# Performance work log

Hardware: AMD Instinct MI355X
Metric: run time of the kernel (lower is better)

The kernel has to match this reference:

```python
import math
import jax, jax.numpy as jnp
import numpy as np

NUM_HEAD = 8
EPS = 1e-5

def _ln(v, w, b):
    m = jnp.mean(v, axis=-1, keepdims=True)
    var = jnp.var(v, axis=-1, keepdims=True)  # biased var, as torch LayerNorm
    return (v - m) * jax.lax.rsqrt(var + EPS) * w + b

def setup_inputs() -> dict:
    key = jax.random.key(0)
    ks = jax.random.split(key, 5)
    B, T, D, L, Hd = 16, 2048, 512, 768, 512
    return {
        "x": jax.random.normal(ks[0], (B, T, D), jnp.float32),
        "xf": jax.random.normal(ks[1], (B, T, L), jnp.float32),
        "norm_w": jnp.ones((D,), jnp.float32),
        "norm_b": jnp.zeros((D,), jnp.float32),
        "tnorm_w": jnp.ones((L,), jnp.float32),
        "tnorm_b": jnp.zeros((L,), jnp.float32),
        "Wq": jax.random.normal(ks[2], (Hd, D), jnp.float32) * (1.0 / math.sqrt(D)),
        "Wk": jax.random.normal(ks[3], (Hd, L), jnp.float32) * (1.0 / math.sqrt(L)),
        "Wv": jax.random.normal(ks[4], (Hd, L), jnp.float32) * (1.0 / math.sqrt(L)),
    }

def reference(x, xf, norm_w, norm_b, tnorm_w, tnorm_b, Wq, Wk, Wv):
    B, T, _ = x.shape
    Hd = Wq.shape[0]
    H = NUM_HEAD
    d = Hd // H
    q = _ln(x, norm_w, norm_b) @ Wq.T                 # B,T,Hd
    xf_n = _ln(xf, tnorm_w, tnorm_b)
    k = xf_n @ Wk.T                                   # B,T,Hd (N == T)
    v = xf_n @ Wv.T                                   # B,T,Hd
    qh = q.reshape(B, T, H, d)
    kh = k.reshape(B, T, H, d)
    vh = v.reshape(B, T, H, d)
    # per-position, per-head dot product gate (no softmax)
    w = jnp.einsum('bthd,bthd->bth', qh, kh) / math.sqrt(d)
    # dropout in eval mode = identity
    y2 = (w[..., None] * vh).reshape(B, T, Hd)
    y1 = ((1.0 - w)[..., None] * qh).reshape(B, T, Hd)
    return (y1, y2)
```

## Files before the change

kernel.cpp:

```cpp
#include <hip/hip_runtime.h>

#define NT 512
#define MT 64

typedef __attribute__((ext_vector_type(8))) short short8;
typedef __attribute__((ext_vector_type(4))) float f32x4;
typedef __attribute__((ext_vector_type(4))) unsigned short u16x4;

__device__ __forceinline__ unsigned short f2bf(float f) {
  unsigned int u = __builtin_bit_cast(unsigned int, f);
  u += 0x7fffu + ((u >> 16) & 1u);
  return (unsigned short)(u >> 16);
}

__global__ void cvt_weights(const float* __restrict__ wq,
                            const float* __restrict__ wk,
                            const float* __restrict__ wv,
                            unsigned short* __restrict__ o) {
  int stride = gridDim.x * blockDim.x;
  int i0 = blockIdx.x * blockDim.x + threadIdx.x;
  for (int t = i0; t < 32768; t += stride) {
    int lane = t & 63, n = (t >> 6) & 3, kk32 = (t >> 8) & 15, head = t >> 12;
    int row = head * 64 + n * 16 + (lane & 15);
    int k   = kk32 * 32 + (lane >> 4) * 8;
    const float* s = wq + (size_t)row * 512 + k;
    unsigned short* d = o + (size_t)t * 8;
    #pragma unroll
    for (int e = 0; e < 8; ++e) d[e] = f2bf(s[e]);
  }
  for (int t = i0; t < 49152; t += stride) {
    int lane = t & 63, n = (t >> 6) & 3, rem = t >> 8;
    int kk32 = rem % 24, head = rem / 24;
    int row = head * 64 + n * 16 + (lane & 15);
    int k   = kk32 * 32 + (lane >> 4) * 8;
    const float* s = wk + (size_t)row * 768 + k;
    unsigned short* d = o + 262144 + (size_t)t * 8;
    #pragma unroll
    for (int e = 0; e < 8; ++e) d[e] = f2bf(s[e]);
  }
  for (int t = i0; t < 49152; t += stride) {
    int lane = t & 63, n = (t >> 6) & 3, rem = t >> 8;
    int kk32 = rem % 24, head = rem / 24;
    int row = head * 64 + n * 16 + (lane & 15);
    int k   = kk32 * 32 + (lane >> 4) * 8;
    const float* s = wv + (size_t)row * 768 + k;
    unsigned short* d = o + 655360 + (size_t)t * 8;
    #pragma unroll
    for (int e = 0; e < 8; ++e) d[e] = f2bf(s[e]);
  }
}

__global__ __launch_bounds__(NT, 2)
void fused_xattn(const float* __restrict__ x, const float* __restrict__ xf,
                 const float* __restrict__ nw, const float* __restrict__ nb,
                 const float* __restrict__ tw, const float* __restrict__ tb,
                 const unsigned short* __restrict__ wbf,
                 float* __restrict__ out) {
  __shared__ __attribute__((aligned(16))) char smem[98304];
  const int tid   = threadIdx.x;
  const int lane  = tid & 63;
  const int wid   = tid >> 6;
  const int lr    = lane & 15;
  const int lkb   = (lane >> 4) * 8;
  const int lrow4 = (lane >> 4) * 4;

  const long row0 = (long)blockIdx.x * MT;
  float* __restrict__ y1 = out;
  float* __restrict__ y2 = out + 16777216L;

  {
    f32x4 t0[8], t1[8];
    #pragma unroll
    for (int j = 0; j < 8; ++j) {
      const f32x4* rp = (const f32x4*)(x + (row0 + wid + 8 * j) * 512);
      t0[j] = rp[lane]; t1[j] = rp[lane + 64];
    }
    const f32x4* g4 = (const f32x4*)nw;
    const f32x4* b4 = (const f32x4*)nb;
    f32x4 g0 = g4[lane], g1 = g4[lane + 64];
    f32x4 c0 = b4[lane], c1 = b4[lane + 64];
    #pragma unroll
    for (int j = 0; j < 8; ++j) {
      f32x4 a = t0[j], b = t1[j];
      float s  = a.x + a.y + a.z + a.w + b.x + b.y + b.z + b.w;
      float s2 = a.x*a.x + a.y*a.y + a.z*a.z + a.w*a.w
               + b.x*b.x + b.y*b.y + b.z*b.z + b.w*b.w;
      #pragma unroll
      for (int m = 1; m < 64; m <<= 1) { s += __shfl_xor(s, m, 64); s2 += __shfl_xor(s2, m, 64); }
      float mean = s * (1.0f / 512.0f);
      float var  = s2 * (1.0f / 512.0f) - mean * mean;
      float rs   = rsqrtf(var + 1e-5f);
      u16x4 o0 = { f2bf((a.x - mean) * rs * g0.x + c0.x),
                   f2bf((a.y - mean) * rs * g0.y + c0.y),
                   f2bf((a.z - mean) * rs * g0.z + c0.z),
                   f2bf((a.w - mean) * rs * g0.w + c0.w) };
      u16x4 o1 = { f2bf((b.x - mean) * rs * g1.x + c1.x),
                   f2bf((b.y - mean) * rs * g1.y + c1.y),
                   f2bf((b.z - mean) * rs * g1.z + c1.z),
                   f2bf((b.w - mean) * rs * g1.w + c1.w) };
      int r = wid + 8 * j;
      int base = r * 1024, sw = (r & 7) << 4;
      *(u16x4*)(smem + ((base +       lane * 8) ^ sw)) = o0;
      *(u16x4*)(smem + ((base + 512 + lane * 8) ^ sw)) = o1;
    }
  }
  __syncthreads();

  f32x4 fr0[8], fr1[8], fr2[8];
  #pragma unroll
  for (int j = 0; j < 8; ++j) {
    const f32x4* rp = (const f32x4*)(xf + (row0 + wid + 8 * j) * 768);
    fr0[j] = rp[lane]; fr1[j] = rp[lane + 64]; fr2[j] = rp[lane + 128];
  }

  f32x4 qa[4][4] = {};
  {
    const unsigned short* bq = wbf + wid * 32768 + lane * 8;
    short8 bc[4], ac[4];
    #pragma unroll
    for (int n = 0; n < 4; ++n) bc[n] = *(const short8*)(bq + n * 512);
    #pragma unroll
    for (int m = 0; m < 4; ++m) {
      int row = m * 16 + lr;
      ac[m] = *(const short8*)(smem + ((row * 1024 + lkb * 2) ^ ((row & 7) << 4)));
    }
    for (int kk = 0; kk < 16; ++kk) {
      short8 bn[4], an[4];
      if (kk < 15) {
        #pragma unroll
        for (int n = 0; n < 4; ++n)
          bn[n] = *(const short8*)(bq + (kk + 1) * 2048 + n * 512);
        #pragma unroll
        for (int m = 0; m < 4; ++m) {
          int row = m * 16 + lr;
          an[m] = *(const short8*)(smem + ((row * 1024 + ((kk + 1) * 32 + lkb) * 2) ^ ((row & 7) << 4)));
        }
      }
      #pragma unroll
      for (int n = 0; n < 4; ++n)
        #pragma unroll
        for (int m = 0; m < 4; ++m)
          qa[m][n] = __builtin_amdgcn_mfma_f32_16x16x32_bf16(ac[m], bc[n], qa[m][n], 0, 0, 0);
      if (kk < 15) {
        #pragma unroll
        for (int n = 0; n < 4; ++n) bc[n] = bn[n];
        #pragma unroll
        for (int m = 0; m < 4; ++m) ac[m] = an[m];
      }
    }
  }
  __syncthreads();

  {
    const f32x4* g4 = (const f32x4*)tw;
    const f32x4* b4 = (const f32x4*)tb;
    f32x4 g0 = g4[lane], g1 = g4[lane + 64], g2 = g4[lane + 128];
    f32x4 c0 = b4[lane], c1 = b4[lane + 64], c2 = b4[lane + 128];
    #pragma unroll
    for (int j = 0; j < 8; ++j) {
      f32x4 a = fr0[j], b = fr1[j], c = fr2[j];
      float s  = a.x + a.y + a.z + a.w + b.x + b.y + b.z + b.w
               + c.x + c.y + c.z + c.w;
      float s2 = a.x*a.x + a.y*a.y + a.z*a.z + a.w*a.w
               + b.x*b.x + b.y*b.y + b.z*b.z + b.w*b.w
               + c.x*c.x + c.y*c.y + c.z*c.z + c.w*c.w;
      #pragma unroll
      for (int m = 1; m < 64; m <<= 1) { s += __shfl_xor(s, m, 64); s2 += __shfl_xor(s2, m, 64); }
      float mean = s * (1.0f / 768.0f);
      float var  = s2 * (1.0f / 768.0f) - mean * mean;
      float rs   = rsqrtf(var + 1e-5f);
      u16x4 o0 = { f2bf((a.x - mean) * rs * g0.x + c0.x),
                   f2bf((a.y - mean) * rs * g0.y + c0.y),
                   f2bf((a.z - mean) * rs * g0.z + c0.z),
                   f2bf((a.w - mean) * rs * g0.w + c0.w) };
      u16x4 o1 = { f2bf((b.x - mean) * rs * g1.x + c1.x),
                   f2bf((b.y - mean) * rs * g1.y + c1.y),
                   f2bf((b.z - mean) * rs * g1.z + c1.z),
                   f2bf((b.w - mean) * rs * g1.w + c1.w) };
      u16x4 o2 = { f2bf((c.x - mean) * rs * g2.x + c2.x),
                   f2bf((c.y - mean) * rs * g2.y + c2.y),
                   f2bf((c.z - mean) * rs * g2.z + c2.z),
                   f2bf((c.w - mean) * rs * g2.w + c2.w) };
      int r = wid + 8 * j;
      int base = r * 1536, sw = (r & 7) << 4;
      *(u16x4*)(smem + ((base +        lane * 8) ^ sw)) = o0;
      *(u16x4*)(smem + ((base + 512  + lane * 8) ^ sw)) = o1;
      *(u16x4*)(smem + ((base + 1024 + lane * 8) ^ sw)) = o2;
    }
  }
  __syncthreads();

  f32x4 ka[4][4] = {};
  {
    const unsigned short* bk = wbf + 262144 + wid * 49152 + lane * 8;
    short8 bc[4], ac[4];
    #pragma unroll
    for (int n = 0; n < 4; ++n) bc[n] = *(const short8*)(bk + n * 512);
    #pragma unroll
    for (int m = 0; m < 4; ++m) {
      int row = m * 16 + lr;
      ac[m] = *(const short8*)(smem + ((row * 1536 + lkb * 2) ^ ((row & 7) << 4)));
    }
    for (int kk = 0; kk < 24; ++kk) {
      short8 bn[4], an[4];
      if (kk < 23) {
        #pragma unroll
        for (int n = 0; n < 4; ++n)
          bn[n] = *(const short8*)(bk + (kk + 1) * 2048 + n * 512);
        #pragma unroll
        for (int m = 0; m < 4; ++m) {
          int row = m * 16 + lr;
          an[m] = *(const short8*)(smem + ((row * 1536 + ((kk + 1) * 32 + lkb) * 2) ^ ((row & 7) << 4)));
        }
      }
      #pragma unroll
      for (int n = 0; n < 4; ++n)
        #pragma unroll
        for (int m = 0; m < 4; ++m)
          ka[m][n] = __builtin_amdgcn_mfma_f32_16x16x32_bf16(ac[m], bc[n], ka[m][n], 0, 0, 0);
      if (kk < 23) {
        #pragma unroll
        for (int n = 0; n < 4; ++n) bc[n] = bn[n];
        #pragma unroll
        for (int m = 0; m < 4; ++m) ac[m] = an[m];
      }
    }
  }

  float wgt[4][4];
  #pragma unroll
  for (int m = 0; m < 4; ++m) {
    #pragma unroll
    for (int r = 0; r < 4; ++r) {
      float p = 0.0f;
      #pragma unroll
      for (int n = 0; n < 4; ++n) p += qa[m][n][r] * ka[m][n][r];
      #pragma unroll
      for (int msk = 1; msk < 16; msk <<= 1) p += __shfl_xor(p, msk, 64);
      wgt[m][r] = p * 0.125f;
    }
  }
  #pragma unroll
  for (int m = 0; m < 4; ++m) {
    #pragma unroll
    for (int r = 0; r < 4; ++r) {
      float f = 1.0f - wgt[m][r];
      long grow = row0 + m * 16 + lrow4 + r;
      #pragma unroll
      for (int n = 0; n < 4; ++n) {
        int ch = wid * 64 + n * 16 + lr;
        y1[grow * 512 + ch] = f * qa[m][n][r];
      }
    }
  }

  f32x4 va[4][4] = {};
  {
    const unsigned short* bv = wbf + 655360 + wid * 49152 + lane * 8;
    short8 bc[4], ac[4];
    #pragma unroll
    for (int n = 0; n < 4; ++n) bc[n] = *(const short8*)(bv + n * 512);
    #pragma unroll
    for (int m = 0; m < 4; ++m) {
      int row = m * 16 + lr;
      ac[m] = *(const short8*)(smem + ((row * 1536 + lkb * 2) ^ ((row & 7) << 4)));
    }
    for (int kk = 0; kk < 24; ++kk) {
      short8 bn[4], an[4];
      if (kk < 23) {
        #pragma unroll
        for (int n = 0; n < 4; ++n)
          bn[n] = *(const short8*)(bv + (kk + 1) * 2048 + n * 512);
        #pragma unroll
        for (int m = 0; m < 4; ++m) {
          int row = m * 16 + lr;
          an[m] = *(const short8*)(smem + ((row * 1536 + ((kk + 1) * 32 + lkb) * 2) ^ ((row & 7) << 4)));
        }
      }
      #pragma unroll
      for (int n = 0; n < 4; ++n)
        #pragma unroll
        for (int m = 0; m < 4; ++m)
          va[m][n] = __builtin_amdgcn_mfma_f32_16x16x32_bf16(ac[m], bc[n], va[m][n], 0, 0, 0);
      if (kk < 23) {
        #pragma unroll
        for (int n = 0; n < 4; ++n) bc[n] = bn[n];
        #pragma unroll
        for (int m = 0; m < 4; ++m) ac[m] = an[m];
      }
    }
  }
  #pragma unroll
  for (int m = 0; m < 4; ++m) {
    #pragma unroll
    for (int r = 0; r < 4; ++r) {
      float f = wgt[m][r];
      long grow = row0 + m * 16 + lrow4 + r;
      #pragma unroll
      for (int n = 0; n < 4; ++n) {
        int ch = wid * 64 + n * 16 + lr;
        y2[grow * 512 + ch] = f * va[m][n][r];
      }
    }
  }
}

extern "C" void kernel_launch(void* const* d_in, const int* in_sizes, int n_in,
                              void* d_out, int out_size, void* d_ws, size_t ws_size,
                              hipStream_t stream) {
  const float* x  = (const float*)d_in[0];
  const float* xf = (const float*)d_in[1];
  const float* nw = (const float*)d_in[2];
  const float* nb = (const float*)d_in[3];
  const float* tw = (const float*)d_in[4];
  const float* tb = (const float*)d_in[5];
  const float* wq = (const float*)d_in[6];
  const float* wk = (const float*)d_in[7];
  const float* wv = (const float*)d_in[8];
  unsigned short* wbf = (unsigned short*)d_ws;

  cvt_weights<<<256, 256, 0, stream>>>(wq, wk, wv, wbf);
  fused_xattn<<<512, NT, 0, stream>>>(x, xf, nw, nb, tw, tb, wbf, (float*)d_out);
}
```

Before: 117.2 us.

## Fuse K and V GEMMs, spill Q to LDS as bf16, chunk LayerNorm loads

Splits shared memory into separate buffers for normalized x and xf. The xf LayerNorm now runs in chunks with loads prefetched between chunks, interleaved after the Q GEMM. The K and V GEMMs are merged into one loop that shares A-fragment LDS reads, and the Q accumulators are parked in LDS as bf16 to free registers. This cuts LDS traffic and register pressure, but total LDS grows to 160KB per block, which likely limits occupancy to one block per CU, and q is rounded to bf16 in y1 and the gate, adding precision error.

After: 125.5 us. +7.1%, slower.

```diff
diff --git a/kernel.cpp b/kernel.cpp
--- a/kernel.cpp
+++ b/kernel.cpp
@@ -11,6 +11,9 @@
   unsigned int u = __builtin_bit_cast(unsigned int, f);
   u += 0x7fffu + ((u >> 16) & 1u);
   return (unsigned short)(u >> 16);
+}
+__device__ __forceinline__ float bf2f(unsigned short h) {
+  return __builtin_bit_cast(float, ((unsigned int)h) << 16);
 }
 
 __global__ void cvt_weights(const float* __restrict__ wq,
@@ -56,7 +59,8 @@
                  const float* __restrict__ tw, const float* __restrict__ tb,
                  const unsigned short* __restrict__ wbf,
                  float* __restrict__ out) {
-  __shared__ __attribute__((aligned(16))) char smem[98304];
+  __shared__ __attribute__((aligned(16))) char ldsX[65536];
+  __shared__ __attribute__((aligned(16))) char ldsF[98304];
   const int tid   = threadIdx.x;
   const int lane  = tid & 63;
   const int wid   = tid >> 6;
@@ -69,164 +73,219 @@
   float* __restrict__ y2 = out + 16777216L;
 
   {
-    f32x4 t0[8], t1[8];
-    #pragma unroll
-    for (int j = 0; j < 8; ++j) {
-      const f32x4* rp = (const f32x4*)(x + (row0 + wid + 8 * j) * 512);
-      t0[j] = rp[lane]; t1[j] = rp[lane + 64];
-    }
     const f32x4* g4 = (const f32x4*)nw;
     const f32x4* b4 = (const f32x4*)nb;
     f32x4 g0 = g4[lane], g1 = g4[lane + 64];
     f32x4 c0 = b4[lane], c1 = b4[lane + 64];
     #pragma unroll
-    for (int j = 0; j < 8; ++j) {
-      f32x4 a = t0[j], b = t1[j];
-      float s  = a.x + a.y + a.z + a.w + b.x + b.y + b.z + b.w;
-      float s2 = a.x*a.x + a.y*a.y + a.z*a.z + a.w*a.w
-               + b.x*b.x + b.y*b.y + b.z*b.z + b.w*b.w;
-      #pragma unroll
-      for (int m = 1; m < 64; m <<= 1) { s += __shfl_xor(s, m, 64); s2 += __shfl_xor(s2, m, 64); }
-      float mean = s * (1.0f / 512.0f);
-      float var  = s2 * (1.0f / 512.0f) - mean * mean;
-      float rs   = rsqrtf(var + 1e-5f);
-      u16x4 o0 = { f2bf((a.x - mean) * rs * g0.x + c0.x),
-                   f2bf((a.y - mean) * rs * g0.y + c0.y),
-                   f2bf((a.z - mean) * rs * g0.z + c0.z),
-                   f2bf((a.w - mean) * rs * g0.w + c0.w) };
-      u16x4 o1 = { f2bf((b.x - mean) * rs * g1.x + c1.x),
-                   f2bf((b.y - mean) * rs * g1.y + c1.y),
-                   f2bf((b.z - mean) * rs * g1.z + c1.z),
-                   f2bf((b.w - mean) * rs * g1.w + c1.w) };
-      int r = wid + 8 * j;
-      int base = r * 1024, sw = (r & 7) << 4;
-      *(u16x4*)(smem + ((base +       lane * 8) ^ sw)) = o0;
-      *(u16x4*)(smem + ((base + 512 + lane * 8) ^ sw)) = o1;
+    for (int cch = 0; cch < 2; ++cch) {
+      f32x4 t0[4], t1[4];
+      #pragma unroll
+      for (int j = 0; j < 4; ++j) {
+        const f32x4* rp = (const f32x4*)(x + (row0 + wid + 8 * (cch * 4 + j)) * 512);
+        t0[j] = rp[lane]; t1[j] = rp[lane + 64];
+      }
+      #pragma unroll
+      for (int j = 0; j < 4; ++j) {
+        f32x4 a = t0[j], b = t1[j];
+        float s  = a.x + a.y + a.z + a.w + b.x + b.y + b.z + b.w;
+        float s2 = a.x*a.x + a.y*a.y + a.z*a.z + a.w*a.w
+                 + b.x*b.x + b.y*b.y + b.z*b.z + b.w*b.w;
+        #pragma unroll
+        for (int m = 1; m < 64; m <<= 1) { s += __shfl_xor(s, m, 64); s2 += __shfl_xor(s2, m, 64); }
+        float mean = s * (1.0f / 512.0f);
+        float var  = s2 * (1.0f / 512.0f) - mean * mean;
+        float rs   = rsqrtf(var + 1e-5f);
+        u16x4 o0 = { f2bf((a.x - mean) * rs * g0.x + c0.x),
+                     f2bf((a.y - mean) * rs * g0.y + c0.y),
+                     f2bf((a.z - mean) * rs * g0.z + c0.z),
+                     f2bf((a.w - mean) * rs * g0.w + c0.w) };
+        u16x4 o1 = { f2bf((b.x - mean) * rs * g1.x + c1.x),
+                     f2bf((b.y - mean) * rs * g1.y + c1.y),
+                     f2bf((b.z - mean) * rs * g1.z + c1.z),
+                     f2bf((b.w - mean) * rs * g1.w + c1.w) };
+        int r = wid + 8 * (cch * 4 + j);
+        int base = r * 1024, sw = (r & 7) << 4;
+        *(u16x4*)(ldsX + ((base +       lane * 8) ^ sw)) = o0;
+        *(u16x4*)(ldsX + ((base + 512 + lane * 8) ^ sw)) = o1;
+      }
     }
   }
   __syncthreads();
 
-  f32x4 fr0[8], fr1[8], fr2[8];
+  f32x4 f0[2], f1[2], f2[2];
   #pragma unroll
-  for (int j = 0; j < 8; ++j) {
+  for (int j = 0; j < 2; ++j) {
     const f32x4* rp = (const f32x4*)(xf + (row0 + wid + 8 * j) * 768);
-    fr0[j] = rp[lane]; fr1[j] = rp[lane + 64]; fr2[j] = rp[lane + 128];
+    f0[j] = rp[lane]; f1[j] = rp[lane + 64]; f2[j] = rp[lane + 128];
   }
 
   f32x4 qa[4][4] = {};
   {
     const unsigned short* bq = wbf + wid * 32768 + lane * 8;
-    short8 bc[4], ac[4];
+    short8 bc[4];
     #pragma unroll
     for (int n = 0; n < 4; ++n) bc[n] = *(const short8*)(bq + n * 512);
-    #pragma unroll
-    for (int m = 0; m < 4; ++m) {
-      int row = m * 16 + lr;
-      ac[m] = *(const short8*)(smem + ((row * 1024 + lkb * 2) ^ ((row & 7) << 4)));
-    }
     for (int kk = 0; kk < 16; ++kk) {
-      short8 bn[4], an[4];
+      short8 a[4];
+      #pragma unroll
+      for (int m = 0; m < 4; ++m) {
+        int row = m * 16 + lr;
+        a[m] = *(const short8*)(ldsX + ((row * 1024 + (kk * 32 + lkb) * 2) ^ ((row & 7) << 4)));
+      }
+      short8 bn[4];
       if (kk < 15) {
         #pragma unroll
-        for (int n = 0; n < 4; ++n)
-          bn[n] = *(const short8*)(bq + (kk + 1) * 2048 + n * 512);
+        for (int n = 0; n < 4; ++n) bn[n] = *(const short8*)(bq + (kk + 1) * 2048 + n * 512);
+      }
+      #pragma unroll
+      for (int n = 0; n < 4; ++n)
+        #pragma unroll
+        for (int m = 0; m < 4; ++m)
+          qa[m][n] = __builtin_amdgcn_mfma_f32_16x16x32_bf16(a[m], bc[n], qa[m][n], 0, 0, 0);
+      if (kk < 15) {
+        #pragma unroll
+        for (int n = 0; n < 4; ++n) bc[n] = bn[n];
+      }
+    }
+  }
+
+  const f32x4* tg4 = (const f32x4*)tw;
+  const f32x4* tb4 = (const f32x4*)tb;
+  f32x4 tg0 = tg4[lane], tg1 = tg4[lane + 64], tg2 = tg4[lane + 128];
+  f32x4 tc0 = tb4[lane], tc1 = tb4[lane + 64], tc2 = tb4[lane + 128];
+
+#define LNF_CHUNK(c2)                                                          \
+  {                                                                            \
+    _Pragma("unroll")                                                          \
+    for (int j = 0; j < 2; ++j) {                                              \
+      f32x4 a = f0[j], b = f1[j], c = f2[j];                                   \
+      float s  = a.x + a.y + a.z + a.w + b.x + b.y + b.z + b.w                 \
+               + c.x + c.y + c.z + c.w;                                        \
+      float s2 = a.x*a.x + a.y*a.y + a.z*a.z + a.w*a.w                         \
+               + b.x*b.x + b.y*b.y + b.z*b.z + b.w*b.w                         \
+               + c.x*c.x + c.y*c.y + c.z*c.z + c.w*c.w;                        \
+      _Pragma("unroll")                                                        \
+      for (int m = 1; m < 64; m <<= 1) {                                       \
+        s += __shfl_xor(s, m, 64); s2 += __shfl_xor(s2, m, 64);                \
+      }                                                                        \
+      float mean = s * (1.0f / 768.0f);                                        \
+      float var  = s2 * (1.0f / 768.0f) - mean * mean;                         \
+      float rs   = rsqrtf(var + 1e-5f);                                        \
+      u16x4 o0 = { f2bf((a.x - mean) * rs * tg0.x + tc0.x),                    \
+                   f2bf((a.y - mean) * rs * tg0.y + tc0.y),                    \
+                   f2bf((a.z - mean) * rs * tg0.z + tc0.z),                    \
+                   f2bf((a.w - mean) * rs * tg0.w + tc0.w) };                  \
+      u16x4 o1 = { f2bf((b.x - mean) * rs * tg1.x + tc1.x),                    \
+                   f2bf((b.y - mean) * rs * tg1.y + tc1.y),                    \
+                   f2bf((b.z - mean) * rs * tg1.z + tc1.z),                    \
+                   f2bf((b.w - mean) * rs * tg1.w + tc1.w) };                  \
+      u16x4 o2 = { f2bf((c.x - mean) * rs * tg2.x + tc2.x),                    \
+                   f2bf((c.y - mean) * rs * tg2.y + tc2.y),                    \
+                   f2bf((c.z - mean) * rs * tg2.z + tc2.z),                    \
+                   f2bf((c.w - mean) * rs * tg2.w + tc2.w) };                  \
+      int r = wid + 8 * ((c2) * 2 + j);                                        \
+      int base = r * 1536, sw = (r & 7) << 4;                                  \
+      *(u16x4*)(ldsF + ((base +        lane * 8) ^ sw)) = o0;                  \
+      *(u16x4*)(ldsF + ((base + 512  + lane * 8) ^ sw)) = o1;                  \
+      *(u16x4*)(ldsF + ((base + 1024 + lane * 8) ^ sw)) = o2;                  \
+    }                                                                          \
+  }
+#define LDF_CHUNK(c2)                                                          \
+  {                                                                            \
+    _Pragma("unroll")                                                          \
+    for (int j = 0; j < 2; ++j) {                                              \
+      const f32x4* rp = (const f32x4*)(xf + (row0 + wid + 8 * ((c2) * 2 + j)) * 768); \
+      f0[j] = rp[lane]; f1[j] = rp[lane + 64]; f2[j] = rp[lane + 128];         \
+    }                                                                          \
+  }
+
+  {
+    f32x4 n0[2], n1[2], n2[2];
+    #pragma unroll
+    for (int j = 0; j < 2; ++j) {
+      const f32x4* rp = (const f32x4*)(xf + (row0 + wid + 8 * (2 + j)) * 768);
+      n0[j] = rp[lane]; n1[j] = rp[lane + 64]; n2[j] = rp[lane + 128];
+    }
+    LNF_CHUNK(0)
+    #pragma unroll
+    for (int j = 0; j < 2; ++j) { f0[j] = n0[j]; f1[j] = n1[j]; f2[j] = n2[j]; }
+  }
+  __syncthreads();
+
+  {
+    unsigned long long* q8 = (unsigned long long*)ldsX;
+    #pragma unroll
+    for (int m = 0; m < 4; ++m)
+      #pragma unroll
+      for (int n = 0; n < 4; ++n) {
+        unsigned long long v =
+            (unsigned long long)f2bf(qa[m][n][0])
+          | ((unsigned long long)f2bf(qa[m][n][1]) << 16)
+          | ((unsigned long long)f2bf(qa[m][n][2]) << 32)
+          | ((unsigned long long)f2bf(qa[m][n][3]) << 48);
+        q8[wid * 1024 + (m * 4 + n) * 64 + lane] = v;
+      }
+  }
+
+  {
+    f32x4 n0[2], n1[2], n2[2];
+    #pragma unroll
+    for (int j = 0; j < 2; ++j) {
+      const f32x4* rp = (const f32x4*)(xf + (row0 + wid + 8 * (4 + j)) * 768);
+      n0[j] = rp[lane]; n1[j] = rp[lane + 64]; n2[j] = rp[lane + 128];
+    }
+    LNF_CHUNK(1)
+    #pragma unroll
+    for (int j = 0; j < 2; ++j) { f0[j] = n0[j]; f1[j] = n1[j]; f2[j] = n2[j]; }
+    #pragma unroll
+    for (int j = 0; j < 2; ++j) {
+      const f32x4* rp = (const f32x4*)(xf + (row0 + wid + 8 * (6 + j)) * 768);
+      n0[j] = rp[lane]; n1[j] = rp[lane + 64]; n2[j] = rp[lane + 128];
+    }
+    LNF_CHUNK(2)
+    #pragma unroll
+    for (int j = 0; j < 2; ++j) { f0[j] = n0[j]; f1[j] = n1[j]; f2[j] = n2[j]; }
+    LNF_CHUNK(3)
+  }
+  __syncthreads();
+
+  f32x4 ka[4][4] = {}, va[4][4] = {};
+  {
+    const unsigned short* bk = wbf + 262144 + wid * 49152 + lane * 8;
+    const unsigned short* bv = wbf + 655360 + wid * 49152 + lane * 8;
+    for (int kk = 0; kk < 24; ++kk) {
+      short8 kf[4], vf[4];
+      #pragma unroll
+      for (int n = 0; n < 4; ++n) {
+        kf[n] = *(const short8*)(bk + kk * 2048 + n * 512);
+        vf[n] = *(const short8*)(bv + kk * 2048 + n * 512);
+      }
+      short8 a[4];
+      #pragma unroll
+      for (int m = 0; m < 4; ++m) {
+        int row = m * 16 + lr;
+        a[m] = *(const short8*)(ldsF + ((row * 1536 + (kk * 32 + lkb) * 2) ^ ((row & 7) << 4)));
+      }
+      #pragma unroll
+      for (int n = 0; n < 4; ++n)
         #pragma unroll
         for (int m = 0; m < 4; ++m) {
-          int row = m * 16 + lr;
-          an[m] = *(const short8*)(smem + ((row * 1024 + ((kk + 1) * 32 + lkb) * 2) ^ ((row & 7) << 4)));
+          ka[m][n] = __builtin_amdgcn_mfma_f32_16x16x32_bf16(a[m], kf[n], ka[m][n], 0, 0, 0);
+          va[m][n] = __builtin_amdgcn_mfma_f32_16x16x32_bf16(a[m], vf[n], va[m][n], 0, 0, 0);
         }
-      }
+    }
+  }
+
+  unsigned long long q64[4][4];
+  {
+    const unsigned long long* q8 = (const unsigned long long*)ldsX;
+    #pragma unroll
+    for (int m = 0; m < 4; ++m)
       #pragma unroll
       for (int n = 0; n < 4; ++n)
-        #pragma unroll
-        for (int m = 0; m < 4; ++m)
-          qa[m][n] = __builtin_amdgcn_mfma_f32_16x16x32_bf16(ac[m], bc[n], qa[m][n], 0, 0, 0);
-      if (kk < 15) {
-        #pragma unroll
-        for (int n = 0; n < 4; ++n) bc[n] = bn[n];
-        #pragma unroll
-        for (int m = 0; m < 4; ++m) ac[m] = an[m];
-      }
-    }
-  }
-  __syncthreads();
-
-  {
-    const f32x4* g4 = (const f32x4*)tw;
-    const f32x4* b4 = (const f32x4*)tb;
-    f32x4 g0 = g4[lane], g1 = g4[lane + 64], g2 = g4[lane + 128];
-    f32x4 c0 = b4[lane], c1 = b4[lane + 64], c2 = b4[lane + 128];
-    #pragma unroll
-    for (int j = 0; j < 8; ++j) {
-      f32x4 a = fr0[j], b = fr1[j], c = fr2[j];
-      float s  = a.x + a.y + a.z + a.w + b.x + b.y + b.z + b.w
-               + c.x + c.y + c.z + c.w;
-      float s2 = a.x*a.x + a.y*a.y + a.z*a.z + a.w*a.w
-               + b.x*b.x + b.y*b.y + b.z*b.z + b.w*b.w
-               + c.x*c.x + c.y*c.y + c.z*c.z + c.w*c.w;
-      #pragma unroll
-      for (int m = 1; m < 64; m <<= 1) { s += __shfl_xor(s, m, 64); s2 += __shfl_xor(s2, m, 64); }
-      float mean = s * (1.0f / 768.0f);
-      float var  = s2 * (1.0f / 768.0f) - mean * mean;
-      float rs   = rsqrtf(var + 1e-5f);
-      u16x4 o0 = { f2bf((a.x - mean) * rs * g0.x + c0.x),
-                   f2bf((a.y - mean) * rs * g0.y + c0.y),
-                   f2bf((a.z - mean) * rs * g0.z + c0.z),
-                   f2bf((a.w - mean) * rs * g0.w + c0.w) };
-      u16x4 o1 = { f2bf((b.x - mean) * rs * g1.x + c1.x),
-                   f2bf((b.y - mean) * rs * g1.y + c1.y),
-                   f2bf((b.z - mean) * rs * g1.z + c1.z),
-                   f2bf((b.w - mean) * rs * g1.w + c1.w) };
-      u16x4 o2 = { f2bf((c.x - mean) * rs * g2.x + c2.x),
-                   f2bf((c.y - mean) * rs * g2.y + c2.y),
-                   f2bf((c.z - mean) * rs * g2.z + c2.z),
-                   f2bf((c.w - mean) * rs * g2.w + c2.w) };
-      int r = wid + 8 * j;
-      int base = r * 1536, sw = (r & 7) << 4;
-      *(u16x4*)(smem + ((base +        lane * 8) ^ sw)) = o0;
-      *(u16x4*)(smem + ((base + 512  + lane * 8) ^ sw)) = o1;
-      *(u16x4*)(smem + ((base + 1024 + lane * 8) ^ sw)) = o2;
-    }
-  }
-  __syncthreads();
-
-  f32x4 ka[4][4] = {};
-  {
-    const unsigned short* bk = wbf + 262144 + wid * 49152 + lane * 8;
-    short8 bc[4], ac[4];
-    #pragma unroll
-    for (int n = 0; n < 4; ++n) bc[n] = *(const short8*)(bk + n * 512);
-    #pragma unroll
-    for (int m = 0; m < 4; ++m) {
-      int row = m * 16 + lr;
-      ac[m] = *(const short8*)(smem + ((row * 1536 + lkb * 2) ^ ((row & 7) << 4)));
-    }
-    for (int kk = 0; kk < 24; ++kk) {
-      short8 bn[4], an[4];
-      if (kk < 23) {
-        #pragma unroll
-        for (int n = 0; n < 4; ++n)
-          bn[n] = *(const short8*)(bk + (kk + 1) * 2048 + n * 512);
-        #pragma unroll
-        for (int m = 0; m < 4; ++m) {
-          int row = m * 16 + lr;
-          an[m] = *(const short8*)(smem + ((row * 1536 + ((kk + 1) * 32 + lkb) * 2) ^ ((row & 7) << 4)));
-        }
-      }
-      #pragma unroll
-      for (int n = 0; n < 4; ++n)
-        #pragma unroll
-        for (int m = 0; m < 4; ++m)
-          ka[m][n] = __builtin_amdgcn_mfma_f32_16x16x32_bf16(ac[m], bc[n], ka[m][n], 0, 0, 0);
-      if (kk < 23) {
-        #pragma unroll
-        for (int n = 0; n < 4; ++n) bc[n] = bn[n];
-        #pragma unroll
-        for (int m = 0; m < 4; ++m) ac[m] = an[m];
-      }
-    }
-  }
-
+        q64[m][n] = q8[wid * 1024 + (m * 4 + n) * 64 + lane];
+  }
   float wgt[4][4];
   #pragma unroll
   for (int m = 0; m < 4; ++m) {
@@ -234,7 +293,8 @@
     for (int r = 0; r < 4; ++r) {
       float p = 0.0f;
       #pragma unroll
-      for (int n = 0; n < 4; ++n) p += qa[m][n][r] * ka[m][n][r];
+      for (int n = 0; n < 4; ++n)
+        p += bf2f((unsigned short)(q64[m][n] >> (16 * r))) * ka[m][n][r];
       #pragma unroll
       for (int msk = 1; msk < 16; msk <<= 1) p += __shfl_xor(p, msk, 64);
       wgt[m][r] = p * 0.125f;
@@ -249,44 +309,7 @@
       #pragma unroll
       for (int n = 0; n < 4; ++n) {
         int ch = wid * 64 + n * 16 + lr;
-        y1[grow * 512 + ch] = f * qa[m][n][r];
-      }
-    }
-  }
-
-  f32x4 va[4][4] = {};
-  {
-    const unsigned short* bv = wbf + 655360 + wid * 49152 + lane * 8;
-    short8 bc[4], ac[4];
-    #pragma unroll
-    for (int n = 0; n < 4; ++n) bc[n] = *(const short8*)(bv + n * 512);
-    #pragma unroll
-    for (int m = 0; m < 4; ++m) {
-      int row = m * 16 + lr;
-      ac[m] = *(const short8*)(smem + ((row * 1536 + lkb * 2) ^ ((row & 7) << 4)));
-    }
-    for (int kk = 0; kk < 24; ++kk) {
-      short8 bn[4], an[4];
-      if (kk < 23) {
-        #pragma unroll
-        for (int n = 0; n < 4; ++n)
-          bn[n] = *(const short8*)(bv + (kk + 1) * 2048 + n * 512);
-        #pragma unroll
-        for (int m = 0; m < 4; ++m) {
-          int row = m * 16 + lr;
-          an[m] = *(const short8*)(smem + ((row * 1536 + ((kk + 1) * 32 + lkb) * 2) ^ ((row & 7) << 4)));
-        }
-      }
-      #pragma unroll
-      for (int n = 0; n < 4; ++n)
-        #pragma unroll
-        for (int m = 0; m < 4; ++m)
-          va[m][n] = __builtin_amdgcn_mfma_f32_16x16x32_bf16(ac[m], bc[n], va[m][n], 0, 0, 0);
-      if (kk < 23) {
-        #pragma unroll
-        for (int n = 0; n < 4; ++n) bc[n] = bn[n];
-        #pragma unroll
-        for (int m = 0; m < 4; ++m) ac[m] = an[m];
+        y1[grow * 512 + ch] = f * bf2f((unsigned short)(q64[m][n] >> (16 * r)));
       }
     }
   }
@@ -303,6 +326,8 @@
       }
     }
   }
+#undef LNF_CHUNK
+#undef LDF_CHUNK
 }
 
 extern "C" void kernel_launch(void* const* d_in, const int* in_sizes, int n_in,
```
